# Performance work log

Measured on AMD Instinct MI355X. Metric: run time of the kernel, lower is better.

Reference implementation:

```python
import jax, jax.numpy as jnp
import numpy as np

# module-level constants from the original repo
NUM_CLASSES = 4
CLASS_NONE = 0
RETINA_SIZE = 224.0

# loss weights (ContourLoss defaults)
POINT_W, ORIENT_W, CLASS_W, INTERSECT_W = 1.0, 0.5, 1.0, 0.1

B, S = 8, 2048


def setup_inputs() -> dict:
    key = jax.random.key(0)
    k1, k2, k3, k4, k5, k6, k7 = jax.random.split(key, 7)
    point_pred = jax.random.uniform(k1, (B, S, 2), jnp.float32) * RETINA_SIZE
    orient_pred = jax.random.normal(k2, (B, S, 2), jnp.float32)
    orient_pred = orient_pred / jnp.linalg.norm(orient_pred, axis=-1, keepdims=True)
    class_pred = jax.random.normal(k3, (B, S, NUM_CLASSES), jnp.float32)
    tgt_pts = jax.random.uniform(k4, (B, S, 2), jnp.float32) * RETINA_SIZE
    tgt_orient = jax.random.normal(k5, (B, S, 2), jnp.float32)
    tgt_orient = tgt_orient / jnp.linalg.norm(tgt_orient, axis=-1, keepdims=True)
    tgt_cls = jax.random.randint(k6, (B, S), 0, NUM_CLASSES).astype(jnp.float32)
    target_seq = jnp.concatenate([tgt_pts, tgt_orient, tgt_cls[..., None]], axis=-1)
    padding_mask = jax.random.bernoulli(k7, 0.15, (B, S))
    return {"point_pred": point_pred, "orient_pred": orient_pred,
            "class_pred": class_pred, "target_seq": target_seq,
            "padding_mask": padding_mask}


def _intersection_per_sample(pts, non_none):
    # pts: (S,2), non_none: (S,) bool.
    # Compact valid points to the front (stable), mirroring point_pred[b, valid_idx].
    order = jnp.argsort(jnp.logical_not(non_none), stable=True)
    pts_c = pts[order]                      # (S,2), first n rows valid
    n = non_none.sum()
    n_seg = n - 1
    starts, ends = pts_c[:-1], pts_c[1:]    # (S-1,2)
    M = S - 1
    ii = jnp.arange(M)[:, None]
    jj = jnp.arange(M)[None, :]
    mask = ((jj >= ii + 2) & (ii < n_seg) & (jj < n_seg)
            & ~((ii == 0) & (jj == n_seg - 1)) & (n >= 4))
    p1 = starts[:, None, :]; p2 = ends[:, None, :]   # segment i
    p3 = starts[None, :, :]; p4 = ends[None, :, :]   # segment j

    def cross(a, b, c):
        return ((b[..., 0] - a[..., 0]) * (c[..., 1] - a[..., 1])
                - (b[..., 1] - a[..., 1]) * (c[..., 0] - a[..., 0]))

    d1 = cross(p3, p4, p1)
    d2 = cross(p3, p4, p2)
    d3 = cross(p1, p2, p3)
    d4 = cross(p1, p2, p4)
    s = jax.nn.sigmoid(-d1 * d2 * 0.01) * jax.nn.sigmoid(-d3 * d4 * 0.01)
    return jnp.where(mask, s, 0.0).sum(), mask.sum()


def reference(point_pred, orient_pred, class_pred, target_seq, padding_mask):
    Bd, Sd, _ = class_pred.shape
    target_class = target_seq[:, :, 4].astype(jnp.int32)
    target_point = target_seq[:, :, :2]
    target_orient = target_seq[:, :, 2:4]
    valid = jnp.logical_not(padding_mask)
    valid_f = valid.astype(jnp.float32)

    # classification: cross entropy, masked mean over valid tokens
    logp = jax.nn.log_softmax(class_pred, axis=-1)
    cls = -jnp.take_along_axis(logp, target_class[..., None], axis=-1)[..., 0]
    cls_loss = (cls * valid_f).sum() / jnp.maximum(valid_f.sum(), 1.0)

    non_none = valid & (target_class != CLASS_NONE)
    nn_f = non_none.astype(jnp.float32)
    nn_denom = jnp.maximum(nn_f.sum(), 1.0)

    # point: SmoothL1 (beta=1) on normalized coords, mean over xy, masked mean
    d = (point_pred - target_point) / RETINA_SIZE
    ad = jnp.abs(d)
    sl1 = jnp.where(ad < 1.0, 0.5 * d * d, ad - 0.5).mean(axis=-1)
    pt_loss = (sl1 * nn_f).sum() / nn_denom

    # orientation: 1 - cosine similarity (orient_pred assumed L2-normalized)
    cos_sim = (orient_pred * target_orient).sum(axis=-1)
    orient_loss = ((1.0 - cos_sim) * nn_f).sum() / nn_denom

    # intersection penalty over non-adjacent segment pairs, per sample
    sums, counts = jax.vmap(_intersection_per_sample)(point_pred, non_none)
    cnt = counts.sum()
    intersect_loss = jnp.where(cnt > 0, sums.sum() / jnp.maximum(cnt, 1).astype(jnp.float32), 0.0)

    total = (POINT_W * pt_loss + ORIENT_W * orient_loss
             + CLASS_W * cls_loss + INTERSECT_W * intersect_loss)
    return (total, pt_loss, orient_loss, cls_loss, intersect_loss)
```

## Files before the change

### kernel.cpp

```cpp
#include <hip/hip_runtime.h>

#define B 8
#define S 2048
#define NBPS 128
#define NBLK_INTER (B * NBPS)
#define NBLK_LOSS 64
#define NBLK_TOTAL (NBLK_INTER + NBLK_LOSS + 1)
#define TPB 256
#define MAGIC 0xA5C97E31u

typedef unsigned long long ull;
typedef unsigned int uint;

__device__ __forceinline__ void slot_store(ull* p, uint payload) {
    __hip_atomic_store(p, ((ull)MAGIC << 32) | (ull)payload,
                       __ATOMIC_RELAXED, __HIP_MEMORY_SCOPE_AGENT);
}
__device__ __forceinline__ uint slot_wait(ull* p) {
    ull w;
    do {
        w = __hip_atomic_load(p, __ATOMIC_RELAXED, __HIP_MEMORY_SCOPE_AGENT);
    } while ((uint)(w >> 32) != MAGIC);
    return (uint)w;
}
__device__ __forceinline__ void slot_clear(ull* p) {
    __hip_atomic_store(p, 0ull, __ATOMIC_RELAXED, __HIP_MEMORY_SCOPE_AGENT);
}

__global__ __launch_bounds__(TPB) void mega_kernel(
    const float2* __restrict__ point_pred,
    const float2* __restrict__ orient_pred,
    const float4* __restrict__ class_pred,
    const float*  __restrict__ target_seq,
    const int*    __restrict__ padding_mask,
    ull* __restrict__ slots,
    float* __restrict__ out)
{
    __shared__ float2 sp[S];
    __shared__ float red[TPB / 64][5];
    __shared__ int wsum[TPB / 64], woff[TPB / 64], nTot;

    ull* sp_partial = slots;
    ull* sp_acc     = slots + NBLK_INTER;
    ull* sp_nbuf    = slots + NBLK_INTER + 5 * NBLK_LOSS;

    const int blk = blockIdx.x;
    const int tid = threadIdx.x;
    const int lane = tid & 63, wv = tid >> 6;

    if (blk < NBLK_INTER) {
        const int b = blk >> 7;
        const int iblk = blk & (NBPS - 1);
        const int base = b * S;
        const int e0 = tid * 8;

        const int4* pm4 = (const int4*)(padding_mask + base + e0);
        const int4 ma = pm4[0], mb = pm4[1];
        const float4* tr4 = (const float4*)(target_seq + (size_t)(base + e0) * 5);
        float4 tq[10];
        #pragma unroll
        for (int k = 0; k < 10; ++k) tq[k] = tr4[k];
        float t4v[8];
        t4v[0] = tq[1].x; t4v[1] = tq[2].y; t4v[2] = tq[3].z; t4v[3] = tq[4].w;
        t4v[4] = tq[6].x; t4v[5] = tq[7].y; t4v[6] = tq[8].z; t4v[7] = tq[9].w;
        const float4* pq4 = (const float4*)(point_pred + base + e0);
        const float4 pa = pq4[0], pb = pq4[1], pc = pq4[2], pd = pq4[3];
        float2 p[8];
        p[0] = make_float2(pa.x, pa.y); p[1] = make_float2(pa.z, pa.w);
        p[2] = make_float2(pb.x, pb.y); p[3] = make_float2(pb.z, pb.w);
        p[4] = make_float2(pc.x, pc.y); p[5] = make_float2(pc.z, pc.w);
        p[6] = make_float2(pd.x, pd.y); p[7] = make_float2(pd.z, pd.w);
        int f[8];
        f[0] = (ma.x == 0 && (int)t4v[0] != 0) ? 1 : 0;
        f[1] = (ma.y == 0 && (int)t4v[1] != 0) ? 1 : 0;
        f[2] = (ma.z == 0 && (int)t4v[2] != 0) ? 1 : 0;
        f[3] = (ma.w == 0 && (int)t4v[3] != 0) ? 1 : 0;
        f[4] = (mb.x == 0 && (int)t4v[4] != 0) ? 1 : 0;
        f[5] = (mb.y == 0 && (int)t4v[5] != 0) ? 1 : 0;
        f[6] = (mb.z == 0 && (int)t4v[6] != 0) ? 1 : 0;
        f[7] = (mb.w == 0 && (int)t4v[7] != 0) ? 1 : 0;

        const int c = f[0]+f[1]+f[2]+f[3]+f[4]+f[5]+f[6]+f[7];
        int inc = c;
        #pragma unroll
        for (int off = 1; off < 64; off <<= 1) {
            int u = __shfl_up(inc, (unsigned)off, 64);
            if (lane >= off) inc += u;
        }
        if (lane == 63) wsum[wv] = inc;
        __syncthreads();
        if (tid == 0) {
            int run = 0;
            #pragma unroll
            for (int w = 0; w < TPB / 64; ++w) { woff[w] = run; run += wsum[w]; }
            nTot = run;
        }
        __syncthreads();
        int pos = woff[wv] + inc - c;
        #pragma unroll
        for (int k = 0; k < 8; ++k) { if (f[k]) sp[pos++] = p[k]; }
        __syncthreads();

        const int n = nTot;
        if (iblk == 0 && tid == 0) slot_store(&sp_nbuf[b], (uint)n);

        float local = 0.f;
        if (n >= 4) {
            const int n_seg = n - 1;
            for (int i = iblk; i < n_seg - 2; i += NBPS) {
                const float2 q1 = sp[i], q2 = sp[i + 1];
                const float e12x = q2.x - q1.x, e12y = q2.y - q1.y;
                const int jmax = (i == 0) ? n_seg - 1 : n_seg;
                for (int j = i + 2 + tid; j < jmax; j += TPB) {
                    const float2 q3 = sp[j], q4 = sp[j + 1];
                    const float e34x = q4.x - q3.x, e34y = q4.y - q3.y;
                    const float ce = e12x * e34y - e12y * e34x;
                    const float rx = q1.x - q3.x, ry = q1.y - q3.y;
                    const float d1 = e34x * ry - e34y * rx;
                    const float d3 = e12y * rx - e12x * ry;
                    const float d2 = d1 - ce;
                    const float d4 = d3 + ce;
                    const float ea = __expf(d1 * d2 * 0.01f);
                    const float eb = __expf(d3 * d4 * 0.01f);
                    local += __builtin_amdgcn_rcpf((1.f + ea) * (1.f + eb));
                }
            }
        }
        #pragma unroll
        for (int off = 32; off > 0; off >>= 1)
            local += __shfl_down(local, (unsigned)off, 64);
        if (lane == 0) red[wv][0] = local;
        __syncthreads();
        if (tid == 0)
            slot_store(&sp_partial[blk],
                       __float_as_uint(red[0][0] + red[1][0] + red[2][0] + red[3][0]));
    } else if (blk < NBLK_INTER + NBLK_LOSS) {
        const int lb = blk - NBLK_INTER;
        const int idx = lb * TPB + tid;
        const bool valid = (padding_mask[idx] == 0);
        const float t4 = target_seq[(size_t)idx * 5 + 4];
        const int tc = (int)t4;
        const bool nn = valid && (tc != 0);
        float cls_a = 0.f, pt_a = 0.f, or_a = 0.f, v_a = 0.f, nn_a = 0.f;
        if (valid) {
            const float4 cl = class_pred[idx];
            const float m = fmaxf(fmaxf(cl.x, cl.y), fmaxf(cl.z, cl.w));
            const float lse = m + logf(expf(cl.x - m) + expf(cl.y - m) +
                                       expf(cl.z - m) + expf(cl.w - m));
            const float ct = (tc == 0) ? cl.x : (tc == 1) ? cl.y : (tc == 2) ? cl.z : cl.w;
            cls_a = lse - ct;
            v_a = 1.f;
        }
        if (nn) {
            const float2 pp = point_pred[idx];
            const float tx = target_seq[(size_t)idx * 5 + 0];
            const float ty = target_seq[(size_t)idx * 5 + 1];
            const float dx = (pp.x - tx) * (1.0f / 224.0f);
            const float dy = (pp.y - ty) * (1.0f / 224.0f);
            const float adx = fabsf(dx), ady = fabsf(dy);
            const float l0 = (adx < 1.f) ? 0.5f * dx * dx : adx - 0.5f;
            const float l1 = (ady < 1.f) ? 0.5f * dy * dy : ady - 0.5f;
            pt_a = 0.5f * (l0 + l1);
            const float2 op = orient_pred[idx];
            const float ox = target_seq[(size_t)idx * 5 + 2];
            const float oy = target_seq[(size_t)idx * 5 + 3];
            or_a = 1.f - (op.x * ox + op.y * oy);
            nn_a = 1.f;
        }
        #pragma unroll
        for (int off = 32; off > 0; off >>= 1) {
            cls_a += __shfl_down(cls_a, (unsigned)off, 64);
            pt_a  += __shfl_down(pt_a,  (unsigned)off, 64);
            or_a  += __shfl_down(or_a,  (unsigned)off, 64);
            v_a   += __shfl_down(v_a,   (unsigned)off, 64);
            nn_a  += __shfl_down(nn_a,  (unsigned)off, 64);
        }
        if (lane == 0) {
            red[wv][0] = cls_a; red[wv][1] = pt_a; red[wv][2] = or_a;
            red[wv][3] = v_a;   red[wv][4] = nn_a;
        }
        __syncthreads();
        if (tid == 0) {
            #pragma unroll
            for (int c5 = 0; c5 < 5; ++c5)
                slot_store(&sp_acc[c5 * NBLK_LOSS + lb],
                           __float_as_uint(red[0][c5] + red[1][c5] +
                                           red[2][c5] + red[3][c5]));
        }
    } else {
        float s = 0.f;
        #pragma unroll
        for (int k = 0; k < 4; ++k)
            s += __uint_as_float(slot_wait(&sp_partial[tid + TPB * k]));
        #pragma unroll
        for (int off = 32; off > 0; off >>= 1)
            s += __shfl_down(s, (unsigned)off, 64);
        if (lane == 0) red[wv][0] = s;
        __syncthreads();
        const float inter_sum = red[0][0] + red[1][0] + red[2][0] + red[3][0];

        float a[5] = {0.f, 0.f, 0.f, 0.f, 0.f};
        if (wv == 0) {
            #pragma unroll
            for (int ch = 0; ch < 5; ++ch)
                a[ch] = __uint_as_float(slot_wait(&sp_acc[ch * NBLK_LOSS + lane]));
            #pragma unroll
            for (int off = 32; off > 0; off >>= 1) {
                #pragma unroll
                for (int ch = 0; ch < 5; ++ch)
                    a[ch] += __shfl_down(a[ch], (unsigned)off, 64);
            }
        }

        if (tid == 0) {
            long long cnt = 0;
            #pragma unroll
            for (int b2 = 0; b2 < B; ++b2) {
                const int n = (int)slot_wait(&sp_nbuf[b2]);
                if (n >= 4) {
                    const long long ns = n - 1;
                    cnt += (ns - 1) * (ns - 2) / 2 - 1;
                }
            }
            const float cls_loss = a[0] / fmaxf(a[3], 1.f);
            const float pt_loss = a[1] / fmaxf(a[4], 1.f);
            const float orient_loss = a[2] / fmaxf(a[4], 1.f);
            const float intersect_loss = (cnt > 0) ? inter_sum / (float)cnt : 0.f;
            out[0] = 1.0f * pt_loss + 0.5f * orient_loss +
                     1.0f * cls_loss + 0.1f * intersect_loss;
            out[1] = pt_loss;
            out[2] = orient_loss;
            out[3] = cls_loss;
            out[4] = intersect_loss;
        }

        #pragma unroll
        for (int k = 0; k < 4; ++k) slot_clear(&sp_partial[tid + TPB * k]);
        if (wv == 0) {
            #pragma unroll
            for (int ch = 0; ch < 5; ++ch) slot_clear(&sp_acc[ch * NBLK_LOSS + lane]);
        }
        if (tid == 0) {
            #pragma unroll
            for (int b2 = 0; b2 < B; ++b2) slot_clear(&sp_nbuf[b2]);
        }
    }
}

extern "C" void kernel_launch(void* const* d_in, const int* in_sizes, int n_in,
                              void* d_out, int out_size, void* d_ws, size_t ws_size,
                              hipStream_t stream) {
    (void)in_sizes; (void)n_in; (void)out_size; (void)ws_size;
    const float2* point_pred  = (const float2*)d_in[0];
    const float2* orient_pred = (const float2*)d_in[1];
    const float4* class_pred  = (const float4*)d_in[2];
    const float*  target_seq  = (const float*)d_in[3];
    const int*    padding_mask = (const int*)d_in[4];

    mega_kernel<<<NBLK_TOTAL, TPB, 0, stream>>>(point_pred, orient_pred,
                                                class_pred, target_seq,
                                                padding_mask,
                                                (ull*)d_ws, (float*)d_out);
}
```

Measured before the change: 21.76 us.

## Make cross-block reduction hierarchical via per-batch master blocks

The first intersection block of each batch now spin-waits on the other 127 partials for that batch, reduces them and publishes one per-batch sum together with the valid-point count. The final block then waits only on 8 batch sums and 320 loss slots, spread across all its threads, instead of 1024 partials. Slot clearing moves to the consumers. This shortens the serial tail in the finalizing block. In exchange it adds a second dependent wait stage, and it relies on all blocks being co-resident, since master blocks spin on blocks launched after them.

```diff
diff --git a/kernel.cpp b/kernel.cpp
--- a/kernel.cpp
+++ b/kernel.cpp
@@ -37,12 +37,13 @@
     float* __restrict__ out)
 {
     __shared__ float2 sp[S];
-    __shared__ float red[TPB / 64][5];
+    __shared__ float redf[TPB / 64][5];
     __shared__ int wsum[TPB / 64], woff[TPB / 64], nTot;
 
-    ull* sp_partial = slots;
-    ull* sp_acc     = slots + NBLK_INTER;
-    ull* sp_nbuf    = slots + NBLK_INTER + 5 * NBLK_LOSS;
+    ull* sl_partial = slots;
+    ull* sl_master  = slots + NBLK_INTER;
+    ull* sl_nbuf    = slots + NBLK_INTER + 8;
+    ull* sl_loss    = slots + NBLK_INTER + 16;
 
     const int blk = blockIdx.x;
     const int tid = threadIdx.x;
@@ -102,8 +103,6 @@
         __syncthreads();
 
         const int n = nTot;
-        if (iblk == 0 && tid == 0) slot_store(&sp_nbuf[b], (uint)n);
-
         float local = 0.f;
         if (n >= 4) {
             const int n_seg = n - 1;
@@ -129,11 +128,35 @@
         #pragma unroll
         for (int off = 32; off > 0; off >>= 1)
             local += __shfl_down(local, (unsigned)off, 64);
-        if (lane == 0) red[wv][0] = local;
-        __syncthreads();
-        if (tid == 0)
-            slot_store(&sp_partial[blk],
-                       __float_as_uint(red[0][0] + red[1][0] + red[2][0] + red[3][0]));
+        if (lane == 0) redf[wv][0] = local;
+        __syncthreads();
+
+        if (iblk != 0) {
+            if (tid == 0)
+                slot_store(&sl_partial[blk],
+                           __float_as_uint(redf[0][0] + redf[1][0] +
+                                           redf[2][0] + redf[3][0]));
+        } else {
+            float val = 0.f;
+            if (tid == 0)
+                val = redf[0][0] + redf[1][0] + redf[2][0] + redf[3][0];
+            __syncthreads();
+            if (tid >= 1 && tid < NBPS) {
+                ull* sl = &sl_partial[blk + tid];
+                val = __uint_as_float(slot_wait(sl));
+                slot_clear(sl);
+            }
+            #pragma unroll
+            for (int off = 32; off > 0; off >>= 1)
+                val += __shfl_down(val, (unsigned)off, 64);
+            if (lane == 0) redf[wv][0] = val;
+            __syncthreads();
+            if (tid == 0) {
+                slot_store(&sl_master[b],
+                           __float_as_uint(redf[0][0] + redf[1][0]));
+                slot_store(&sl_nbuf[b], (uint)n);
+            }
+        }
     } else if (blk < NBLK_INTER + NBLK_LOSS) {
         const int lb = blk - NBLK_INTER;
         const int idx = lb * TPB + tid;
@@ -176,55 +199,60 @@
             nn_a  += __shfl_down(nn_a,  (unsigned)off, 64);
         }
         if (lane == 0) {
-            red[wv][0] = cls_a; red[wv][1] = pt_a; red[wv][2] = or_a;
-            red[wv][3] = v_a;   red[wv][4] = nn_a;
+            redf[wv][0] = cls_a; redf[wv][1] = pt_a; redf[wv][2] = or_a;
+            redf[wv][3] = v_a;   redf[wv][4] = nn_a;
         }
         __syncthreads();
         if (tid == 0) {
             #pragma unroll
             for (int c5 = 0; c5 < 5; ++c5)
-                slot_store(&sp_acc[c5 * NBLK_LOSS + lb],
-                           __float_as_uint(red[0][c5] + red[1][c5] +
-                                           red[2][c5] + red[3][c5]));
+                slot_store(&sl_loss[c5 * NBLK_LOSS + lb],
+                           __float_as_uint(redf[0][c5] + redf[1][c5] +
+                                           redf[2][c5] + redf[3][c5]));
         }
     } else {
-        float s = 0.f;
-        #pragma unroll
-        for (int k = 0; k < 4; ++k)
-            s += __uint_as_float(slot_wait(&sp_partial[tid + TPB * k]));
-        #pragma unroll
-        for (int off = 32; off > 0; off >>= 1)
-            s += __shfl_down(s, (unsigned)off, 64);
-        if (lane == 0) red[wv][0] = s;
-        __syncthreads();
-        const float inter_sum = red[0][0] + red[1][0] + red[2][0] + red[3][0];
-
-        float a[5] = {0.f, 0.f, 0.f, 0.f, 0.f};
-        if (wv == 0) {
-            #pragma unroll
-            for (int ch = 0; ch < 5; ++ch)
-                a[ch] = __uint_as_float(slot_wait(&sp_acc[ch * NBLK_LOSS + lane]));
-            #pragma unroll
-            for (int off = 32; off > 0; off >>= 1) {
-                #pragma unroll
-                for (int ch = 0; ch < 5; ++ch)
-                    a[ch] += __shfl_down(a[ch], (unsigned)off, 64);
-            }
-        }
+        __shared__ float fs[B];
+        __shared__ int fn[B];
+        __shared__ float chs[5];
+
+        if (tid < B) {
+            ull* pm = &sl_master[tid];
+            ull* pn = &sl_nbuf[tid];
+            fs[tid] = __uint_as_float(slot_wait(pm)); slot_clear(pm);
+            fn[tid] = (int)slot_wait(pn);             slot_clear(pn);
+        }
+        ull* pl0 = &sl_loss[tid];
+        float lv0 = __uint_as_float(slot_wait(pl0)); slot_clear(pl0);
+        float lv1 = 0.f;
+        if (tid < 64) {
+            ull* pl1 = &sl_loss[256 + tid];
+            lv1 = __uint_as_float(slot_wait(pl1)); slot_clear(pl1);
+        }
+        #pragma unroll
+        for (int off = 32; off > 0; off >>= 1) {
+            lv0 += __shfl_down(lv0, (unsigned)off, 64);
+            lv1 += __shfl_down(lv1, (unsigned)off, 64);
+        }
+        if (lane == 0) chs[wv] = lv0;
+        if (tid == 0) chs[4] = lv1;
+        __syncthreads();
 
         if (tid == 0) {
+            float inter_sum = 0.f;
+            #pragma unroll
+            for (int b2 = 0; b2 < B; ++b2) inter_sum += fs[b2];
             long long cnt = 0;
             #pragma unroll
             for (int b2 = 0; b2 < B; ++b2) {
-                const int n = (int)slot_wait(&sp_nbuf[b2]);
+                const int n = fn[b2];
                 if (n >= 4) {
                     const long long ns = n - 1;
                     cnt += (ns - 1) * (ns - 2) / 2 - 1;
                 }
             }
-            const float cls_loss = a[0] / fmaxf(a[3], 1.f);
-            const float pt_loss = a[1] / fmaxf(a[4], 1.f);
-            const float orient_loss = a[2] / fmaxf(a[4], 1.f);
+            const float cls_loss = chs[0] / fmaxf(chs[3], 1.f);
+            const float pt_loss = chs[1] / fmaxf(chs[4], 1.f);
+            const float orient_loss = chs[2] / fmaxf(chs[4], 1.f);
             const float intersect_loss = (cnt > 0) ? inter_sum / (float)cnt : 0.f;
             out[0] = 1.0f * pt_loss + 0.5f * orient_loss +
                      1.0f * cls_loss + 0.1f * intersect_loss;
@@ -232,17 +260,6 @@
             out[2] = orient_loss;
             out[3] = cls_loss;
             out[4] = intersect_loss;
-        }
-
-        #pragma unroll
-        for (int k = 0; k < 4; ++k) slot_clear(&sp_partial[tid + TPB * k]);
-        if (wv == 0) {
-            #pragma unroll
-            for (int ch = 0; ch < 5; ++ch) slot_clear(&sp_acc[ch * NBLK_LOSS + lane]);
-        }
-        if (tid == 0) {
-            #pragma unroll
-            for (int b2 = 0; b2 < B; ++b2) slot_clear(&sp_nbuf[b2]);
         }
     }
 }
```

New measurement: 19.97 us. 8.2% less time.
